# Performance work log

Measured on AMD Instinct MI355X. Metric: run time of the kernel, lower is better.

## Reference

```python
import jax, jax.numpy as jnp
import numpy as np

N = 100_000   # nodes
E = 1_600_000 # edges
G = 512       # graphs in batch
DIN, DF, DOUT = 78, 32, 128
BN_EPS = 1e-5

def setup_inputs() -> dict:
    key = jax.random.key(0)
    ks = jax.random.split(key, 10)
    s = 0.1
    return {
        "x": jax.random.normal(ks[0], (N, DIN), jnp.float32),
        "edge_index": jax.random.randint(ks[1], (2, E), 0, N, dtype=jnp.int32),
        "batch": jnp.sort(jax.random.randint(ks[2], (N,), 0, G, dtype=jnp.int32)),
        "w1_in": jax.random.normal(ks[3], (DIN, DF), jnp.float32) * s,
        "b1_in": jnp.zeros((DF,), jnp.float32),
        "w1_out": jax.random.normal(ks[4], (DF, DF), jnp.float32) * s,
        "b1_out": jnp.zeros((DF,), jnp.float32),
        "wa": jax.random.normal(ks[5], (4, DF, DF), jnp.float32) * s,
        "ba": jnp.zeros((4, DF), jnp.float32),
        "wb": jax.random.normal(ks[6], (4, DF, DF), jnp.float32) * s,
        "bb": jnp.zeros((4, DF), jnp.float32),
        "gamma": jnp.ones((5, DF), jnp.float32),
        "beta": jnp.zeros((5, DF), jnp.float32),
        "fc_w": jax.random.normal(ks[7], (DF, DOUT), jnp.float32) * s,
        "fc_b": jnp.zeros((DOUT,), jnp.float32),
    }

def _gin_conv(h, src, dst, w1, bv1, w2, bv2):
    # GINConv with eps=0: nn(x + sum_{j in N(i)} x_j)
    agg = jax.ops.segment_sum(h[src], dst, num_segments=N)
    z = h + agg
    return jax.nn.relu(z @ w1 + bv1) @ w2 + bv2

def _bn(h, g, b):
    # BatchNorm1d, training-mode batch statistics (biased variance)
    mu = h.mean(axis=0)
    var = ((h - mu) ** 2).mean(axis=0)
    return g * (h - mu) * jax.lax.rsqrt(var + BN_EPS) + b

def reference(x, edge_index, batch, w1_in, b1_in, w1_out, b1_out,
              wa, ba, wb, bb, gamma, beta, fc_w, fc_b):
    src, dst = edge_index[0], edge_index[1]
    h = _bn(jax.nn.relu(_gin_conv(x, src, dst, w1_in, b1_in, w1_out, b1_out)), gamma[0], beta[0])
    for i in range(4):  # conv2..conv5 (identical shapes)
        h = _bn(jax.nn.relu(_gin_conv(h, src, dst, wa[i], ba[i], wb[i], bb[i])), gamma[i + 1], beta[i + 1])
    pooled = jax.ops.segment_sum(h, batch, num_segments=G)  # global_add_pool -> [G, DF]
    out = jax.nn.relu(pooled @ fc_w + fc_b)
    # dropout omitted (deterministic reference / eval semantics)
    return out
```

## Files before the change

### kernel.cpp

```cpp
#include <hip/hip_runtime.h>
#include <hip/hip_bf16.h>

#define NN 100000
#define EE 1600000
#define GG 512
#define DIN 78
#define DF 32
#define DOUT 128
#define BN_EPS 1e-5f

#define NBLK_NODE 3125

#define SCAN_C 256
#define SCAN_NB ((NN + SCAN_C - 1) / SCAN_C)

__global__ __launch_bounds__(256) void k_hist(const int* __restrict__ dst, int* __restrict__ deg) {
    int e = blockIdx.x * 256 + threadIdx.x;
    if (e < EE) atomicAdd(&deg[dst[e]], 1);
}

__global__ __launch_bounds__(256) void k_scan1(const int* __restrict__ deg, int* __restrict__ bsum) {
    __shared__ int red[256];
    int t = threadIdx.x;
    int i = blockIdx.x * 256 + t;
    red[t] = (i < NN) ? deg[i] : 0;
    __syncthreads();
    for (int off = 128; off > 0; off >>= 1) {
        if (t < off) red[t] += red[t + off];
        __syncthreads();
    }
    if (t == 0) bsum[blockIdx.x] = red[0];
}

__global__ __launch_bounds__(1024) void k_scan2(int* __restrict__ bsum) {
    __shared__ int s[1024];
    int t = threadIdx.x;
    int v = (t < SCAN_NB) ? bsum[t] : 0;
    s[t] = v;
    __syncthreads();
    for (int off = 1; off < 1024; off <<= 1) {
        int u = (t >= off) ? s[t - off] : 0;
        __syncthreads();
        s[t] += u;
        __syncthreads();
    }
    if (t < SCAN_NB) bsum[t] = s[t] - v;
}

__global__ __launch_bounds__(256) void k_scan3(const int* __restrict__ deg, const int* __restrict__ bsum,
                                               int* __restrict__ row_ptr, int* __restrict__ cursor) {
    __shared__ int s[256];
    int t = threadIdx.x;
    int i = blockIdx.x * 256 + t;
    int v = (i < NN) ? deg[i] : 0;
    s[t] = v;
    __syncthreads();
    for (int off = 1; off < 256; off <<= 1) {
        int u = (t >= off) ? s[t - off] : 0;
        __syncthreads();
        s[t] += u;
        __syncthreads();
    }
    int base = bsum[blockIdx.x];
    if (i < NN) {
        int ex = base + s[t] - v;
        row_ptr[i] = ex;
        cursor[i] = ex;
        if (i == NN - 1) row_ptr[NN] = base + s[t];
    }
}

__global__ __launch_bounds__(256) void k_fill(const int* __restrict__ src, const int* __restrict__ dst,
                                              int* __restrict__ cursor, int* __restrict__ col) {
    int e = blockIdx.x * 256 + threadIdx.x;
    if (e < EE) {
        int pos = atomicAdd(&cursor[dst[e]], 1);
        col[pos] = src[e];
    }
}

__global__ __launch_bounds__(256) void k_proj_first(const float* __restrict__ x,
                                                    const float* __restrict__ w1,
                                                    float* __restrict__ p) {
    __shared__ float w[DIN][DF];
    __shared__ float hx[32][DIN];
    int tid = threadIdx.x;
    for (int i = tid; i < DIN * DF; i += 256) w[i >> 5][i & 31] = w1[i];
    int base = blockIdx.x * 32;
    for (int i = tid; i < 32 * DIN; i += 256) hx[i / DIN][i % DIN] = x[base * DIN + i];
    __syncthreads();
    int j = tid & 31;
    #pragma unroll
    for (int it = 0; it < 4; ++it) {
        int rown = (tid >> 5) + 8 * it;
        float acc = 0.f;
        #pragma unroll
        for (int k = 0; k < DIN; ++k) acc += hx[rown][k] * w[k][j];
        p[(base + rown) * DF + j] = acc;
    }
}

__global__ __launch_bounds__(256) void k_proj_hidden(const float* __restrict__ r,
                                                     const float* __restrict__ w1_,
                                                     const float* __restrict__ stats,
                                                     const float* __restrict__ gamma,
                                                     const float* __restrict__ beta,
                                                     float* __restrict__ p) {
    __shared__ float w[DF][DF];
    __shared__ float h[32][DF + 1];
    int tid = threadIdx.x;
    for (int i = tid; i < DF * DF; i += 256) w[i >> 5][i & 31] = w1_[i];
    int grp = tid >> 3, c = tid & 7;
    int node = blockIdx.x * 32 + grp;
    float4 rv  = ((const float4*)r)[node * 8 + c];
    float4 muv = ((const float4*)stats)[c];
    float4 ivv = ((const float4*)(stats + DF))[c];
    float4 gv  = ((const float4*)gamma)[c];
    float4 bv  = ((const float4*)beta)[c];
    h[grp][4 * c + 0] = gv.x * (rv.x - muv.x) * ivv.x + bv.x;
    h[grp][4 * c + 1] = gv.y * (rv.y - muv.y) * ivv.y + bv.y;
    h[grp][4 * c + 2] = gv.z * (rv.z - muv.z) * ivv.z + bv.z;
    h[grp][4 * c + 3] = gv.w * (rv.w - muv.w) * ivv.w + bv.w;
    __syncthreads();
    int j = tid & 31;
    #pragma unroll
    for (int it = 0; it < 4; ++it) {
        int rown = (tid >> 5) + 8 * it;
        float acc = 0.f;
        #pragma unroll
        for (int k = 0; k < DF; ++k) acc += h[rown][k] * w[k][j];
        p[(blockIdx.x * 32 + rown) * DF + j] = acc;
    }
}

__global__ __launch_bounds__(256) void k_agg(const float* __restrict__ p,
                                             const int* __restrict__ row_ptr,
                                             const int* __restrict__ col,
                                             const float* __restrict__ b1,
                                             const float* __restrict__ w2_,
                                             const float* __restrict__ b2,
                                             float* __restrict__ r,
                                             float* __restrict__ partial) {
    __shared__ float w[DF][DF];
    __shared__ float a[32][DF + 1];
    __shared__ float red[4][2][DF];
    int tid = threadIdx.x;
    for (int i = tid; i < DF * DF; i += 256) w[i >> 5][i & 31] = w2_[i];
    int grp = tid >> 3, c = tid & 7;
    int node = blockIdx.x * 32 + grp;
    const float4* p4 = (const float4*)p;
    float4 acc = p4[node * 8 + c];
    int e0 = row_ptr[node], e1 = row_ptr[node + 1];
    for (int e = e0; e < e1; ++e) {
        int srcn = col[e];
        float4 v = p4[srcn * 8 + c];
        acc.x += v.x; acc.y += v.y; acc.z += v.z; acc.w += v.w;
    }
    float4 b1v = ((const float4*)b1)[c];
    a[grp][4 * c + 0] = fmaxf(acc.x + b1v.x, 0.f);
    a[grp][4 * c + 1] = fmaxf(acc.y + b1v.y, 0.f);
    a[grp][4 * c + 2] = fmaxf(acc.z + b1v.z, 0.f);
    a[grp][4 * c + 3] = fmaxf(acc.w + b1v.w, 0.f);
    __syncthreads();
    int j = tid & 31;
    float b2j = b2[j];
    float s1 = 0.f, s2 = 0.f;
    #pragma unroll
    for (int it = 0; it < 4; ++it) {
        int rown = (tid >> 5) + 8 * it;
        float accm = b2j;
        #pragma unroll
        for (int k = 0; k < DF; ++k) accm += a[rown][k] * w[k][j];
        float rv = fmaxf(accm, 0.f);
        r[(blockIdx.x * 32 + rown) * DF + j] = rv;
        s1 += rv;
        s2 += rv * rv;
    }
    s1 += __shfl_down(s1, 32);
    s2 += __shfl_down(s2, 32);
    int wave = tid >> 6, lane = tid & 63;
    if (lane < 32) { red[wave][0][j] = s1; red[wave][1][j] = s2; }
    __syncthreads();
    if (tid < 32) {
        float t1 = red[0][0][j] + red[1][0][j] + red[2][0][j] + red[3][0][j];
        float t2 = red[0][1][j] + red[1][1][j] + red[2][1][j] + red[3][1][j];
        partial[blockIdx.x * 64 + j] = t1;
        partial[blockIdx.x * 64 + 32 + j] = t2;
    }
}

__global__ __launch_bounds__(1024) void k_finalize(const float* __restrict__ partial,
                                                   float* __restrict__ stats) {
    __shared__ double red[32][2][DF];
    int tid = threadIdx.x;
    int g = tid >> 5, j = tid & 31;
    double a1 = 0.0, a2 = 0.0;
    for (int b = g; b < NBLK_NODE; b += 32) {
        a1 += (double)partial[b * 64 + j];
        a2 += (double)partial[b * 64 + 32 + j];
    }
    red[g][0][j] = a1;
    red[g][1][j] = a2;
    __syncthreads();
    if (tid < 32) {
        double s1 = 0.0, s2 = 0.0;
        #pragma unroll
        for (int gg = 0; gg < 32; ++gg) { s1 += red[gg][0][j]; s2 += red[gg][1][j]; }
        double mu = s1 / (double)NN;
        double var = s2 / (double)NN - mu * mu;
        stats[j] = (float)mu;
        stats[DF + j] = (float)(1.0 / sqrt(var + (double)BN_EPS));
    }
}

__global__ __launch_bounds__(256) void k_pool(const float* __restrict__ r,
                                              const float* __restrict__ stats,
                                              const float* __restrict__ gamma,
                                              const float* __restrict__ beta,
                                              const int* __restrict__ batch,
                                              float* __restrict__ pooled) {
    int t = blockIdx.x * 256 + threadIdx.x;
    int nodeBase = (t >> 5) * 8;
    if (nodeBase >= NN) return;
    int j = t & 31;
    float mu = stats[j], inv = stats[DF + j];
    float gj = gamma[j], bj = beta[j];
    float accp = 0.f;
    int curg = batch[nodeBase];
    #pragma unroll
    for (int k = 0; k < 8; ++k) {
        int n = nodeBase + k;
        int g = batch[n];
        float val = gj * (r[n * DF + j] - mu) * inv + bj;
        if (g != curg) { atomicAdd(&pooled[curg * DF + j], accp); accp = 0.f; curg = g; }
        accp += val;
    }
    atomicAdd(&pooled[curg * DF + j], accp);
}

__global__ __launch_bounds__(128) void k_fc(const float* __restrict__ pooled,
                                            const float* __restrict__ fc_w,
                                            const float* __restrict__ fc_b,
                                            float* __restrict__ out) {
    __shared__ float pl[DF];
    int g = blockIdx.x, j = threadIdx.x;
    if (j < DF) pl[j] = pooled[g * DF + j];
    __syncthreads();
    float acc = fc_b[j];
    #pragma unroll
    for (int k = 0; k < DF; ++k) acc += pl[k] * fc_w[k * DOUT + j];
    out[g * DOUT + j] = fmaxf(acc, 0.f);
}

extern "C" void kernel_launch(void* const* d_in, const int* in_sizes, int n_in,
                              void* d_out, int out_size, void* d_ws, size_t ws_size,
                              hipStream_t stream) {
    const float* x      = (const float*)d_in[0];
    const int*   eidx   = (const int*)d_in[1];
    const int*   batch  = (const int*)d_in[2];
    const float* w1_in  = (const float*)d_in[3];
    const float* b1_in  = (const float*)d_in[4];
    const float* w1_out = (const float*)d_in[5];
    const float* b1_out = (const float*)d_in[6];
    const float* wa     = (const float*)d_in[7];
    const float* ba     = (const float*)d_in[8];
    const float* wb     = (const float*)d_in[9];
    const float* bb     = (const float*)d_in[10];
    const float* gamma  = (const float*)d_in[11];
    const float* beta   = (const float*)d_in[12];
    const float* fc_w   = (const float*)d_in[13];
    const float* fc_b   = (const float*)d_in[14];
    float* out = (float*)d_out;

    const int* esrc = eidx;
    const int* edst = eidx + EE;

    float* W = (float*)d_ws;
    float* p       = W;
    float* r       = p + (size_t)NN * DF;
    float* pooled  = r + (size_t)NN * DF;
    float* stats   = pooled + (size_t)GG * DF;
    float* partial = stats + 64;
    int* row_ptr = (int*)(partial + (size_t)NBLK_NODE * 64);
    int* cursor  = row_ptr + (NN + 1);
    int* deg     = cursor + NN;
    int* bsum    = deg + NN;
    int* col     = bsum + SCAN_NB;

    hipMemsetAsync(deg, 0, sizeof(int) * NN, stream);
    k_hist<<<(EE + 255) / 256, 256, 0, stream>>>(edst, deg);
    k_scan1<<<SCAN_NB, 256, 0, stream>>>(deg, bsum);
    k_scan2<<<1, 1024, 0, stream>>>(bsum);
    k_scan3<<<SCAN_NB, 256, 0, stream>>>(deg, bsum, row_ptr, cursor);
    k_fill<<<(EE + 255) / 256, 256, 0, stream>>>(esrc, edst, cursor, col);

    k_proj_first<<<NBLK_NODE, 256, 0, stream>>>(x, w1_in, p);
    k_agg<<<NBLK_NODE, 256, 0, stream>>>(p, row_ptr, col, b1_in, w1_out, b1_out, r, partial);
    k_finalize<<<1, 1024, 0, stream>>>(partial, stats);

    for (int i = 1; i < 5; ++i) {
        const float* w1_ = wa + (size_t)(i - 1) * DF * DF;
        const float* b1_ = ba + (size_t)(i - 1) * DF;
        const float* w2_ = wb + (size_t)(i - 1) * DF * DF;
        const float* b2_ = bb + (size_t)(i - 1) * DF;
        const float* g_  = gamma + (size_t)(i - 1) * DF;
        const float* be_ = beta + (size_t)(i - 1) * DF;
        k_proj_hidden<<<NBLK_NODE, 256, 0, stream>>>(r, w1_, stats, g_, be_, p);
        k_agg<<<NBLK_NODE, 256, 0, stream>>>(p, row_ptr, col, b1_, w2_, b2_, r, partial);
        k_finalize<<<1, 1024, 0, stream>>>(partial, stats);
    }

    hipMemsetAsync(pooled, 0, sizeof(float) * GG * DF, stream);
    k_pool<<<((NN / 8) * 32 + 255) / 256, 256, 0, stream>>>(r, stats, gamma + 4 * DF, beta + 4 * DF,
                                                            batch, pooled);
    k_fc<<<GG, 128, 0, stream>>>(pooled, fc_w, fc_b, out);
}
```

Measured before the change: 893.6 us.

## Build CSR via bucketed two-level sort and fuse BN stats via atomics

The CSR build changes from a global degree histogram, three-pass scan and global-atomic fill to a two-level bucket sort. Edges are first binned by destination into 512-node buckets using shared-memory histograms and scattered as (src,dst) pairs, then each bucket builds its row_ptr and col locally with shared-memory atomics. Separately, the single-block BN finalize kernels are removed: k_agg atomically adds per-block sums straight into per-layer stats buffers, and consumers compute mean and rsqrt inline. The aim is to cut global atomic contention, scattered writes and kernel launches, at the cost of float atomics (nondeterministic summation order) and single-precision variance in place of double.

```diff
diff --git a/kernel.cpp b/kernel.cpp
--- a/kernel.cpp
+++ b/kernel.cpp
@@ -11,71 +11,99 @@
 
 #define NBLK_NODE 3125
 
-#define SCAN_C 256
-#define SCAN_NB ((NN + SCAN_C - 1) / SCAN_C)
-
-__global__ __launch_bounds__(256) void k_hist(const int* __restrict__ dst, int* __restrict__ deg) {
-    int e = blockIdx.x * 256 + threadIdx.x;
-    if (e < EE) atomicAdd(&deg[dst[e]], 1);
-}
-
-__global__ __launch_bounds__(256) void k_scan1(const int* __restrict__ deg, int* __restrict__ bsum) {
-    __shared__ int red[256];
+#define BSH 9
+#define NBUCK 196
+#define SCB 256
+#define EPB (EE / SCB)
+
+__global__ __launch_bounds__(256) void k_bhist(const int* __restrict__ dst, int* __restrict__ hist_g) {
+    __shared__ int hist[NBUCK];
+    int tid = threadIdx.x, blk = blockIdx.x;
+    if (tid < NBUCK) hist[tid] = 0;
+    __syncthreads();
+    int start = blk * EPB, end = start + EPB;
+    for (int i = start + tid; i < end; i += 256) atomicAdd(&hist[dst[i] >> BSH], 1);
+    __syncthreads();
+    if (tid < NBUCK) hist_g[tid * SCB + blk] = hist[tid];
+}
+
+__global__ __launch_bounds__(256) void k_bscan(int* __restrict__ hist_g, int* __restrict__ bbase) {
+    __shared__ int tot[256];
     int t = threadIdx.x;
-    int i = blockIdx.x * 256 + t;
-    red[t] = (i < NN) ? deg[i] : 0;
-    __syncthreads();
-    for (int off = 128; off > 0; off >>= 1) {
-        if (t < off) red[t] += red[t + off];
+    int total = 0;
+    if (t < NBUCK)
+        for (int blk = 0; blk < SCB; ++blk) total += hist_g[t * SCB + blk];
+    tot[t] = (t < NBUCK) ? total : 0;
+    __syncthreads();
+    for (int off = 1; off < 256; off <<= 1) {
+        int u = (t >= off) ? tot[t - off] : 0;
         __syncthreads();
-    }
-    if (t == 0) bsum[blockIdx.x] = red[0];
-}
-
-__global__ __launch_bounds__(1024) void k_scan2(int* __restrict__ bsum) {
-    __shared__ int s[1024];
-    int t = threadIdx.x;
-    int v = (t < SCAN_NB) ? bsum[t] : 0;
-    s[t] = v;
-    __syncthreads();
-    for (int off = 1; off < 1024; off <<= 1) {
-        int u = (t >= off) ? s[t - off] : 0;
+        tot[t] += u;
         __syncthreads();
-        s[t] += u;
+    }
+    int excl = tot[t] - total;
+    if (t < NBUCK) {
+        bbase[t] = excl;
+        int run = excl;
+        for (int blk = 0; blk < SCB; ++blk) {
+            int h = hist_g[t * SCB + blk];
+            hist_g[t * SCB + blk] = run;
+            run += h;
+        }
+    }
+    if (t == 0) bbase[NBUCK] = EE;
+}
+
+__global__ __launch_bounds__(256) void k_bscatter(const int* __restrict__ src, const int* __restrict__ dst,
+                                                  const int* __restrict__ hist_g, int2* __restrict__ pairs) {
+    __shared__ int base_l[NBUCK];
+    __shared__ int cnt[NBUCK];
+    int tid = threadIdx.x, blk = blockIdx.x;
+    if (tid < NBUCK) { base_l[tid] = hist_g[tid * SCB + blk]; cnt[tid] = 0; }
+    __syncthreads();
+    int start = blk * EPB, end = start + EPB;
+    for (int i = start + tid; i < end; i += 256) {
+        int d = dst[i], s = src[i];
+        int b = d >> BSH;
+        int rk = atomicAdd(&cnt[b], 1);
+        pairs[base_l[b] + rk] = make_int2(s, d);
+    }
+}
+
+__global__ __launch_bounds__(256) void k_bfill(const int2* __restrict__ pairs, const int* __restrict__ bbase,
+                                               int* __restrict__ row_ptr, int* __restrict__ col) {
+    __shared__ int cnt[512];
+    __shared__ int excl[512];
+    __shared__ int ps[256];
+    int tid = threadIdx.x, b = blockIdx.x;
+    int base = bbase[b];
+    int cntb = bbase[b + 1] - base;
+    int nbase = b << BSH;
+    int nloc = NN - nbase; if (nloc > 512) nloc = 512;
+    cnt[tid] = 0; cnt[tid + 256] = 0;
+    __syncthreads();
+    for (int i = tid; i < cntb; i += 256) atomicAdd(&cnt[pairs[base + i].y - nbase], 1);
+    __syncthreads();
+    int a0 = cnt[2 * tid], a1 = cnt[2 * tid + 1];
+    ps[tid] = a0 + a1;
+    __syncthreads();
+    for (int off = 1; off < 256; off <<= 1) {
+        int u = (tid >= off) ? ps[tid - off] : 0;
         __syncthreads();
-    }
-    if (t < SCAN_NB) bsum[t] = s[t] - v;
-}
-
-__global__ __launch_bounds__(256) void k_scan3(const int* __restrict__ deg, const int* __restrict__ bsum,
-                                               int* __restrict__ row_ptr, int* __restrict__ cursor) {
-    __shared__ int s[256];
-    int t = threadIdx.x;
-    int i = blockIdx.x * 256 + t;
-    int v = (i < NN) ? deg[i] : 0;
-    s[t] = v;
-    __syncthreads();
-    for (int off = 1; off < 256; off <<= 1) {
-        int u = (t >= off) ? s[t - off] : 0;
+        ps[tid] += u;
         __syncthreads();
-        s[t] += u;
-        __syncthreads();
-    }
-    int base = bsum[blockIdx.x];
-    if (i < NN) {
-        int ex = base + s[t] - v;
-        row_ptr[i] = ex;
-        cursor[i] = ex;
-        if (i == NN - 1) row_ptr[NN] = base + s[t];
-    }
-}
-
-__global__ __launch_bounds__(256) void k_fill(const int* __restrict__ src, const int* __restrict__ dst,
-                                              int* __restrict__ cursor, int* __restrict__ col) {
-    int e = blockIdx.x * 256 + threadIdx.x;
-    if (e < EE) {
-        int pos = atomicAdd(&cursor[dst[e]], 1);
-        col[pos] = src[e];
+    }
+    int pexcl = ps[tid] - (a0 + a1);
+    excl[2 * tid] = pexcl;
+    excl[2 * tid + 1] = pexcl + a0;
+    __syncthreads();
+    for (int i = tid; i < nloc; i += 256) row_ptr[nbase + i] = base + excl[i];
+    if (b == 0 && tid == 0) row_ptr[NN] = EE;
+    __syncthreads();
+    for (int i = tid; i < cntb; i += 256) {
+        int2 pr = pairs[base + i];
+        int lp = atomicAdd(&excl[pr.y - nbase], 1);
+        col[base + lp] = pr.x;
     }
 }
 
@@ -102,7 +130,7 @@
 
 __global__ __launch_bounds__(256) void k_proj_hidden(const float* __restrict__ r,
                                                      const float* __restrict__ w1_,
-                                                     const float* __restrict__ stats,
+                                                     const float* __restrict__ statsL,
                                                      const float* __restrict__ gamma,
                                                      const float* __restrict__ beta,
                                                      float* __restrict__ p) {
@@ -112,15 +140,21 @@
     for (int i = tid; i < DF * DF; i += 256) w[i >> 5][i & 31] = w1_[i];
     int grp = tid >> 3, c = tid & 7;
     int node = blockIdx.x * 32 + grp;
-    float4 rv  = ((const float4*)r)[node * 8 + c];
-    float4 muv = ((const float4*)stats)[c];
-    float4 ivv = ((const float4*)(stats + DF))[c];
+    const float invN = 1.0f / (float)NN;
+    float4 s1v = ((const float4*)statsL)[c];
+    float4 s2v = ((const float4*)(statsL + DF))[c];
     float4 gv  = ((const float4*)gamma)[c];
     float4 bv  = ((const float4*)beta)[c];
-    h[grp][4 * c + 0] = gv.x * (rv.x - muv.x) * ivv.x + bv.x;
-    h[grp][4 * c + 1] = gv.y * (rv.y - muv.y) * ivv.y + bv.y;
-    h[grp][4 * c + 2] = gv.z * (rv.z - muv.z) * ivv.z + bv.z;
-    h[grp][4 * c + 3] = gv.w * (rv.w - muv.w) * ivv.w + bv.w;
+    float4 rv  = ((const float4*)r)[node * 8 + c];
+    float mux = s1v.x * invN, muy = s1v.y * invN, muz = s1v.z * invN, muw = s1v.w * invN;
+    float ivx = rsqrtf(s2v.x * invN - mux * mux + BN_EPS);
+    float ivy = rsqrtf(s2v.y * invN - muy * muy + BN_EPS);
+    float ivz = rsqrtf(s2v.z * invN - muz * muz + BN_EPS);
+    float ivw = rsqrtf(s2v.w * invN - muw * muw + BN_EPS);
+    h[grp][4 * c + 0] = gv.x * (rv.x - mux) * ivx + bv.x;
+    h[grp][4 * c + 1] = gv.y * (rv.y - muy) * ivy + bv.y;
+    h[grp][4 * c + 2] = gv.z * (rv.z - muz) * ivz + bv.z;
+    h[grp][4 * c + 3] = gv.w * (rv.w - muw) * ivw + bv.w;
     __syncthreads();
     int j = tid & 31;
     #pragma unroll
@@ -140,7 +174,7 @@
                                              const float* __restrict__ w2_,
                                              const float* __restrict__ b2,
                                              float* __restrict__ r,
-                                             float* __restrict__ partial) {
+                                             float* __restrict__ statsL) {
     __shared__ float w[DF][DF];
     __shared__ float a[32][DF + 1];
     __shared__ float red[4][2][DF];
@@ -184,37 +218,13 @@
     if (tid < 32) {
         float t1 = red[0][0][j] + red[1][0][j] + red[2][0][j] + red[3][0][j];
         float t2 = red[0][1][j] + red[1][1][j] + red[2][1][j] + red[3][1][j];
-        partial[blockIdx.x * 64 + j] = t1;
-        partial[blockIdx.x * 64 + 32 + j] = t2;
-    }
-}
-
-__global__ __launch_bounds__(1024) void k_finalize(const float* __restrict__ partial,
-                                                   float* __restrict__ stats) {
-    __shared__ double red[32][2][DF];
-    int tid = threadIdx.x;
-    int g = tid >> 5, j = tid & 31;
-    double a1 = 0.0, a2 = 0.0;
-    for (int b = g; b < NBLK_NODE; b += 32) {
-        a1 += (double)partial[b * 64 + j];
-        a2 += (double)partial[b * 64 + 32 + j];
-    }
-    red[g][0][j] = a1;
-    red[g][1][j] = a2;
-    __syncthreads();
-    if (tid < 32) {
-        double s1 = 0.0, s2 = 0.0;
-        #pragma unroll
-        for (int gg = 0; gg < 32; ++gg) { s1 += red[gg][0][j]; s2 += red[gg][1][j]; }
-        double mu = s1 / (double)NN;
-        double var = s2 / (double)NN - mu * mu;
-        stats[j] = (float)mu;
-        stats[DF + j] = (float)(1.0 / sqrt(var + (double)BN_EPS));
+        atomicAdd(&statsL[j], t1);
+        atomicAdd(&statsL[DF + j], t2);
     }
 }
 
 __global__ __launch_bounds__(256) void k_pool(const float* __restrict__ r,
-                                              const float* __restrict__ stats,
+                                              const float* __restrict__ statsL,
                                               const float* __restrict__ gamma,
                                               const float* __restrict__ beta,
                                               const int* __restrict__ batch,
@@ -223,7 +233,9 @@
     int nodeBase = (t >> 5) * 8;
     if (nodeBase >= NN) return;
     int j = t & 31;
-    float mu = stats[j], inv = stats[DF + j];
+    const float invN = 1.0f / (float)NN;
+    float mu = statsL[j] * invN;
+    float inv = rsqrtf(statsL[DF + j] * invN - mu * mu + BN_EPS);
     float gj = gamma[j], bj = beta[j];
     float accp = 0.f;
     int curg = batch[nodeBase];
@@ -280,23 +292,21 @@
     float* r       = p + (size_t)NN * DF;
     float* pooled  = r + (size_t)NN * DF;
     float* stats   = pooled + (size_t)GG * DF;
-    float* partial = stats + 64;
-    int* row_ptr = (int*)(partial + (size_t)NBLK_NODE * 64);
-    int* cursor  = row_ptr + (NN + 1);
-    int* deg     = cursor + NN;
-    int* bsum    = deg + NN;
-    int* col     = bsum + SCAN_NB;
-
-    hipMemsetAsync(deg, 0, sizeof(int) * NN, stream);
-    k_hist<<<(EE + 255) / 256, 256, 0, stream>>>(edst, deg);
-    k_scan1<<<SCAN_NB, 256, 0, stream>>>(deg, bsum);
-    k_scan2<<<1, 1024, 0, stream>>>(bsum);
-    k_scan3<<<SCAN_NB, 256, 0, stream>>>(deg, bsum, row_ptr, cursor);
-    k_fill<<<(EE + 255) / 256, 256, 0, stream>>>(esrc, edst, cursor, col);
+    int* row_ptr = (int*)(stats + 5 * 64);
+    int* col     = row_ptr + (NN + 1);
+    int* hist_g  = col + EE;
+    int* bbase   = hist_g + NBUCK * SCB;
+    int2* pairs  = (int2*)p;
+
+    k_bhist<<<SCB, 256, 0, stream>>>(edst, hist_g);
+    k_bscan<<<1, 256, 0, stream>>>(hist_g, bbase);
+    k_bscatter<<<SCB, 256, 0, stream>>>(esrc, edst, hist_g, pairs);
+    k_bfill<<<NBUCK, 256, 0, stream>>>(pairs, bbase, row_ptr, col);
+
+    hipMemsetAsync(stats, 0, sizeof(float) * 5 * 64, stream);
 
     k_proj_first<<<NBLK_NODE, 256, 0, stream>>>(x, w1_in, p);
-    k_agg<<<NBLK_NODE, 256, 0, stream>>>(p, row_ptr, col, b1_in, w1_out, b1_out, r, partial);
-    k_finalize<<<1, 1024, 0, stream>>>(partial, stats);
+    k_agg<<<NBLK_NODE, 256, 0, stream>>>(p, row_ptr, col, b1_in, w1_out, b1_out, r, stats);
 
     for (int i = 1; i < 5; ++i) {
         const float* w1_ = wa + (size_t)(i - 1) * DF * DF;
@@ -305,13 +315,12 @@
         const float* b2_ = bb + (size_t)(i - 1) * DF;
         const float* g_  = gamma + (size_t)(i - 1) * DF;
         const float* be_ = beta + (size_t)(i - 1) * DF;
-        k_proj_hidden<<<NBLK_NODE, 256, 0, stream>>>(r, w1_, stats, g_, be_, p);
-        k_agg<<<NBLK_NODE, 256, 0, stream>>>(p, row_ptr, col, b1_, w2_, b2_, r, partial);
-        k_finalize<<<1, 1024, 0, stream>>>(partial, stats);
+        k_proj_hidden<<<NBLK_NODE, 256, 0, stream>>>(r, w1_, stats + (i - 1) * 64, g_, be_, p);
+        k_agg<<<NBLK_NODE, 256, 0, stream>>>(p, row_ptr, col, b1_, w2_, b2_, r, stats + i * 64);
     }
 
     hipMemsetAsync(pooled, 0, sizeof(float) * GG * DF, stream);
-    k_pool<<<((NN / 8) * 32 + 255) / 256, 256, 0, stream>>>(r, stats, gamma + 4 * DF, beta + 4 * DF,
-                                                            batch, pooled);
+    k_pool<<<((NN / 8) * 32 + 255) / 256, 256, 0, stream>>>(r, stats + 4 * 64, gamma + 4 * DF,
+                                                            beta + 4 * DF, batch, pooled);
     k_fc<<<GG, 128, 0, stream>>>(pooled, fc_w, fc_b, out);
 }
```

Result: faster. 835.4 us (-6.5%).
